# Optimization experiments

Hardware: AMD Instinct MI355X
Metric: run time of the kernel (lower is better)

## Reference

```python
import jax, jax.numpy as jnp
import numpy as np

B, C, T = 64, 384, 512
DUR_MAX = 8            # durations drawn from [0, 8)
MAX_NEW_TIME = 4096    # static padded output length >= T * (DUR_MAX - 1)


def setup_inputs() -> dict:
    key = jax.random.key(0)
    kx, kd = jax.random.split(key)
    x = jax.random.normal(kx, (B, C, T), dtype=jnp.float32)
    duration = jax.random.randint(kd, (B, 1, T), 0, DUR_MAX, dtype=jnp.int32)
    return {"x": x, "duration": duration}


def reference(x, duration):
    # x: [B, C, T] float32, duration: [B, 1, T] int32
    dur = duration[:, 0, :]                      # [B, T]
    csum = jnp.cumsum(dur, axis=-1)              # [B, T] exclusive-right cumsum boundaries
    total = csum[:, -1]                          # [B] expanded length per sample
    j = jnp.arange(MAX_NEW_TIME, dtype=jnp.int32)  # output frame positions
    # source phoneme index for each output frame: smallest t with j < csum[t]
    idx = jax.vmap(lambda c: jnp.searchsorted(c, j, side="right"))(csum)  # [B, MAX_NEW_TIME]
    idx = jnp.clip(idx, 0, T - 1)
    # gather along time, broadcast over channels -> [B, C, MAX_NEW_TIME]
    out = jnp.take_along_axis(x, idx[:, None, :].astype(jnp.int32), axis=-1)
    valid = j[None, :] < total[:, None]          # [B, MAX_NEW_TIME]
    out = jnp.where(valid[:, None, :], out, jnp.zeros((), dtype=x.dtype))
    # mask derived from non-zero values of channel 0, matching torch code
    new_mask = (out[:, 0:1, :] != 0).astype(jnp.int32)  # [B, 1, MAX_NEW_TIME]
    return out, new_mask
```

## Files before the change

kernel.cpp:

```cpp
#include <hip/hip_runtime.h>


#define BB 64
#define CC 384
#define TT 512
#define TOUT 4096

__global__ __launch_bounds__(TT) void build_idx_kernel(
    const int* __restrict__ dur, int* __restrict__ idx) {
  const int b = blockIdx.x;
  const int t = threadIdx.x;

  __shared__ int s[TT];
  const int d = dur[b * TT + t];
  s[t] = d;
  __syncthreads();

  for (int off = 1; off < TT; off <<= 1) {
    int v = (t >= off) ? s[t - off] : 0;
    __syncthreads();
    s[t] += v;
    __syncthreads();
  }

  const int end = s[t];
  const int start = end - d;

  int* __restrict__ idxb = idx + b * TOUT;
  #pragma unroll
  for (int k = 0; k < TOUT / TT; ++k) idxb[t + k * TT] = -1;
  __syncthreads();

  for (int p = start; p < end; ++p) idxb[p] = t;
}

__global__ __launch_bounds__(256) void gather_kernel(
    const float* __restrict__ x, const int* __restrict__ idx,
    float* __restrict__ out, float* __restrict__ mask) {
  const int b = blockIdx.z;
  const int c = blockIdx.y;
  const int j = (blockIdx.x * 256 + threadIdx.x) * 4;

  const int4 i4 = *(const int4*)(idx + b * TOUT + j);
  const float* __restrict__ xrow = x + ((size_t)b * CC + c) * TT;

  float4 v;
  v.x = (i4.x >= 0) ? xrow[i4.x] : 0.0f;
  v.y = (i4.y >= 0) ? xrow[i4.y] : 0.0f;
  v.z = (i4.z >= 0) ? xrow[i4.z] : 0.0f;
  v.w = (i4.w >= 0) ? xrow[i4.w] : 0.0f;

  *(float4*)(out + (((size_t)b * CC + c) * TOUT) + j) = v;

  if (c == 0) {
    float4 m;
    m.x = (v.x != 0.0f) ? 1.0f : 0.0f;
    m.y = (v.y != 0.0f) ? 1.0f : 0.0f;
    m.z = (v.z != 0.0f) ? 1.0f : 0.0f;
    m.w = (v.w != 0.0f) ? 1.0f : 0.0f;
    *(float4*)(mask + (size_t)b * TOUT + j) = m;
  }
}

extern "C" void kernel_launch(void* const* d_in, const int* in_sizes, int n_in,
                              void* d_out, int out_size, void* d_ws, size_t ws_size,
                              hipStream_t stream) {
  const float* x = (const float*)d_in[0];
  const int* dur = (const int*)d_in[1];

  float* out = (float*)d_out;
  float* mask = out + (size_t)BB * CC * TOUT;

  int* idx = (int*)d_ws;

  build_idx_kernel<<<BB, TT, 0, stream>>>(dur, idx);
  gather_kernel<<<dim3(TOUT / 1024, CC, BB), 256, 0, stream>>>(x, idx, out, mask);
}
```

Measured before the change: 494.7 us.

## Stage channel tiles of x in LDS and reuse indices across channels

Each block now loads 16 channel rows of x for one batch into shared memory and loads the frame-index vector once into registers. It then produces all 4096 output frames for those 16 channels using LDS lookups. This removes the per-channel reloading of indices and the scattered global gathers from x. In exchange it uses 32 KB of LDS per block and a much smaller grid, which may limit occupancy and latency hiding for the store stream.

```diff
diff --git a/kernel.cpp b/kernel.cpp
--- a/kernel.cpp
+++ b/kernel.cpp
@@ -5,6 +5,7 @@
 #define CC 384
 #define TT 512
 #define TOUT 4096
+#define CB 16
 
 __global__ __launch_bounds__(TT) void build_idx_kernel(
     const int* __restrict__ dur, int* __restrict__ idx) {
@@ -37,28 +38,51 @@
 __global__ __launch_bounds__(256) void gather_kernel(
     const float* __restrict__ x, const int* __restrict__ idx,
     float* __restrict__ out, float* __restrict__ mask) {
-  const int b = blockIdx.z;
-  const int c = blockIdx.y;
-  const int j = (blockIdx.x * 256 + threadIdx.x) * 4;
+  const int b = blockIdx.y;
+  const int c0 = blockIdx.x * CB;
+  const int tid = threadIdx.x;
 
-  const int4 i4 = *(const int4*)(idx + b * TOUT + j);
-  const float* __restrict__ xrow = x + ((size_t)b * CC + c) * TT;
+  __shared__ float xs[CB * TT];
 
-  float4 v;
-  v.x = (i4.x >= 0) ? xrow[i4.x] : 0.0f;
-  v.y = (i4.y >= 0) ? xrow[i4.y] : 0.0f;
-  v.z = (i4.z >= 0) ? xrow[i4.z] : 0.0f;
-  v.w = (i4.w >= 0) ? xrow[i4.w] : 0.0f;
+  const float4* __restrict__ xb4 =
+      (const float4*)(x + ((size_t)b * CC + c0) * TT);
+  float4* __restrict__ xs4 = (float4*)xs;
+  #pragma unroll
+  for (int k = 0; k < (CB * TT / 4) / 256; ++k)
+    xs4[k * 256 + tid] = xb4[k * 256 + tid];
 
-  *(float4*)(out + (((size_t)b * CC + c) * TOUT) + j) = v;
+  const int4* __restrict__ ib4 = (const int4*)(idx + (size_t)b * TOUT);
+  int4 I[TOUT / 1024];
+  #pragma unroll
+  for (int jt = 0; jt < TOUT / 1024; ++jt)
+    I[jt] = ib4[jt * 256 + tid];
 
-  if (c == 0) {
-    float4 m;
-    m.x = (v.x != 0.0f) ? 1.0f : 0.0f;
-    m.y = (v.y != 0.0f) ? 1.0f : 0.0f;
-    m.z = (v.z != 0.0f) ? 1.0f : 0.0f;
-    m.w = (v.w != 0.0f) ? 1.0f : 0.0f;
-    *(float4*)(mask + (size_t)b * TOUT + j) = m;
+  __syncthreads();
+
+  float* __restrict__ ob = out + ((size_t)b * CC + c0) * TOUT + tid * 4;
+
+  #pragma unroll
+  for (int c = 0; c < CB; ++c) {
+    const float* __restrict__ xr = xs + c * TT;
+    #pragma unroll
+    for (int jt = 0; jt < TOUT / 1024; ++jt) {
+      const int4 i4 = I[jt];
+      float4 v;
+      v.x = (i4.x >= 0) ? xr[i4.x] : 0.0f;
+      v.y = (i4.y >= 0) ? xr[i4.y] : 0.0f;
+      v.z = (i4.z >= 0) ? xr[i4.z] : 0.0f;
+      v.w = (i4.w >= 0) ? xr[i4.w] : 0.0f;
+      *(float4*)(ob + (size_t)c * TOUT + jt * 1024) = v;
+
+      if (c == 0 && c0 == 0) {
+        float4 m;
+        m.x = (v.x != 0.0f) ? 1.0f : 0.0f;
+        m.y = (v.y != 0.0f) ? 1.0f : 0.0f;
+        m.z = (v.z != 0.0f) ? 1.0f : 0.0f;
+        m.w = (v.w != 0.0f) ? 1.0f : 0.0f;
+        *(float4*)(mask + (size_t)b * TOUT + jt * 1024 + tid * 4) = m;
+      }
+    }
   }
 }
 
@@ -74,5 +98,5 @@
   int* idx = (int*)d_ws;
 
   build_idx_kernel<<<BB, TT, 0, stream>>>(dur, idx);
-  gather_kernel<<<dim3(TOUT / 1024, CC, BB), 256, 0, stream>>>(x, idx, out, mask);
+  gather_kernel<<<dim3(CC / CB, BB), 256, 0, stream>>>(x, idx, out, mask);
 }
```

After: 431.8 us. -12.7%, faster.
